# Optimization experiments

Measured on AMD Instinct MI355X. Metric: run time of the kernel, lower is better.

## Reference

```python
import jax, jax.numpy as jnp
import numpy as np

N_NODES = 50000
N_GRAPHS = 64
HID = 100

def gcn_conv(x, W, b, src, dst, n):
    # dense transform first (PyG GCNConv): [N, out]
    h = x @ W
    # add self loops (improved=False -> fill 1.0)
    loops = jnp.arange(n, dtype=src.dtype)
    s = jnp.concatenate([src, loops])
    d = jnp.concatenate([dst, loops])
    # symmetric normalization D^-1/2 A D^-1/2
    deg = jax.ops.segment_sum(jnp.ones_like(s, dtype=h.dtype), d, num_segments=n)
    dinv = jnp.where(deg > 0, jax.lax.rsqrt(jnp.maximum(deg, 1e-12)), 0.0)
    norm = dinv[s] * dinv[d]  # [E+N]
    msgs = h[s] * norm[:, None]  # gather + scale
    out = jax.ops.segment_sum(msgs, d, num_segments=n)  # scatter-add
    return out + b

def global_mean_pool(x, batch, num_graphs):
    sums = jax.ops.segment_sum(x, batch, num_segments=num_graphs)
    cnts = jax.ops.segment_sum(jnp.ones((x.shape[0],), x.dtype), batch, num_segments=num_graphs)
    return sums / jnp.maximum(cnts, 1.0)[:, None]

def setup_inputs() -> dict:
    key = jax.random.key(0)
    ks = jax.random.split(key, 8)
    d_in = 128
    x = jax.random.normal(ks[0], (N_NODES, d_in), dtype=jnp.float32)
    edge_index = jax.random.randint(ks[1], (2, 800000), 0, N_NODES, dtype=jnp.int64)
    batch = jnp.sort(jax.random.randint(ks[2], (N_NODES,), 0, N_GRAPHS, dtype=jnp.int64))
    s1 = 1.0 / np.sqrt(d_in)
    s2 = 1.0 / np.sqrt(HID)
    W1 = jax.random.uniform(ks[3], (d_in, HID), jnp.float32, -s1, s1)
    b1 = jnp.zeros((HID,), jnp.float32)
    W2 = jax.random.uniform(ks[4], (HID, HID), jnp.float32, -s2, s2)
    b2 = jnp.zeros((HID,), jnp.float32)
    Wlin = jax.random.uniform(ks[5], (HID, 1), jnp.float32, -s2, s2)
    blin = jax.random.uniform(ks[6], (1,), jnp.float32, -s2, s2)
    return {"x": x, "edge_index": edge_index, "batch": batch,
            "W1": W1, "b1": b1, "W2": W2, "b2": b2, "Wlin": Wlin, "blin": blin}

def reference(x, edge_index, batch, W1, b1, W2, b2, Wlin, blin):
    src, dst = edge_index[0], edge_index[1]
    h = gcn_conv(x, W1, b1, src, dst, N_NODES)
    h = jnp.tanh(h)
    h = gcn_conv(h, W2, b2, src, dst, N_NODES)
    g = global_mean_pool(h, batch, N_GRAPHS)  # [G, HID]
    return g @ Wlin + blin  # [G, 1]
```

## Files before the change

### kernel.cpp

```cpp
#include <hip/hip_runtime.h>
#include <hip/hip_bf16.h>

#define N_NODES 50000
#define N_GRAPHS 64
#define HID 100
#define HP 104

#define BKE  4096
#define NBIN 196
#define MAXBLK 256

#define NPB 39

#define OFF_DINV 0
#define OFF_CNTF 50048
#define OFF_POOL 50112
#define OFF_WT1  50176
#define OFF_HS   64512
#define OFF_ROWPTR 7864512
#define OFF_EIDX   7914560
#define OFF_BE     8714560
#define OFF_BBINS  9514560
#define OFF_BOFF   9565760
#define OFF_BTOT   9616960
#define OFF_BBASE  9617216
#define OFF_W2L    9617472
#define OFF_Q      9617600

typedef __attribute__((ext_vector_type(8))) short short8;
typedef __attribute__((ext_vector_type(4))) float floatx4;

__device__ inline float b2f(unsigned int u) {
    union { unsigned int v; float f; } x; x.v = u << 16; return x.f;
}
__device__ inline unsigned short f2b(float f) {
    union { float f; unsigned int v; } x; x.f = f;
    unsigned int r = (x.v + 0x7fffu + ((x.v >> 16) & 1u)) >> 16;
    return (unsigned short)r;
}

__global__ __launch_bounds__(256) void k_prep(const float* __restrict__ W1,
                                              const float* __restrict__ W2,
                                              const float* __restrict__ Wlin,
                                              const float* __restrict__ b2,
                                              unsigned short* __restrict__ Wt1,
                                              float* __restrict__ w2l,
                                              float* __restrict__ pool,
                                              float* __restrict__ cntf) {
    const int b = blockIdx.x, t = threadIdx.x;
    if (b < 56) {
        int idx = b * 256 + t;
        int c = idx >> 7, k = idx & 127;
        float v = (k < 128 && c < HID) ? W1[k * HID + c] : 0.0f;
        Wt1[c * 128 + k] = f2b(v);
    } else {
        if (t < 104) {
            float s = 0.0f;
            if (t < 100)
                for (int c = 0; c < HID; ++c) s += W2[t * HID + c] * Wlin[c];
            w2l[t] = s;
        } else if (t == 104) {
            float s = 0.0f;
            for (int j = 0; j < HID; ++j) s += b2[j] * Wlin[j];
            w2l[104] = s;
        } else if (t >= 128 && t < 128 + N_GRAPHS) {
            pool[t - 128] = 0.0f; cntf[t - 128] = 0.0f;
        }
    }
}

__global__ __launch_bounds__(256) void k_p1(const int* __restrict__ dst, int E,
                                            int* __restrict__ bbins) {
    __shared__ int hist[256];
    const int t = threadIdx.x, b = blockIdx.x;
    hist[t] = 0;
    __syncthreads();
    int e0 = b * BKE, e1 = min(e0 + BKE, E);
    for (int e = e0 + t; e < e1; e += 256) atomicAdd(&hist[dst[e] >> 8], 1);
    __syncthreads();
    if (t < NBIN) bbins[b * NBIN + t] = hist[t];
}

__global__ __launch_bounds__(256) void k_p2a(const int* __restrict__ bbins, int nb,
                                             int* __restrict__ boff, int* __restrict__ btot) {
    __shared__ int sb[256];
    const int t = threadIdx.x, j = blockIdx.x;
    int v = (t < nb) ? bbins[t * NBIN + j] : 0;
    sb[t] = v;
    __syncthreads();
    for (int off = 1; off < 256; off <<= 1) {
        int u = (t >= off) ? sb[t - off] : 0;
        __syncthreads();
        sb[t] += u;
        __syncthreads();
    }
    if (t < nb) boff[t * NBIN + j] = sb[t] - v;
    if (t == 255) btot[j] = sb[255];
}

__global__ __launch_bounds__(256) void k_p2b(const int* __restrict__ btot, int E,
                                             int* __restrict__ bbase, int* __restrict__ rowptr) {
    __shared__ int sb[256];
    const int t = threadIdx.x;
    int v = (t < NBIN) ? btot[t] : 0;
    sb[t] = v;
    __syncthreads();
    for (int off = 1; off < 256; off <<= 1) {
        int u = (t >= off) ? sb[t - off] : 0;
        __syncthreads();
        sb[t] += u;
        __syncthreads();
    }
    if (t < NBIN) bbase[t] = sb[t] - v;
    if (t == 0) { bbase[NBIN] = E; rowptr[N_NODES] = E; }
}

__global__ __launch_bounds__(256) void k_p3(const int* __restrict__ src, const int* __restrict__ dst,
                                            int E, const int* __restrict__ boff,
                                            const int* __restrict__ bbase,
                                            unsigned int* __restrict__ bE) {
    __shared__ unsigned int stage[BKE];
    __shared__ int hist[256], pref[256], cur[256], sb[256], offr[NBIN];
    const int t = threadIdx.x, b = blockIdx.x;
    hist[t] = 0;
    if (t < NBIN) offr[t] = boff[b * NBIN + t] + bbase[t];
    __syncthreads();
    const int e0 = b * BKE, e1 = min(e0 + BKE, E), n = e1 - e0;
    unsigned int mine[16];
#pragma unroll
    for (int u = 0; u < 16; ++u) {
        int e = e0 + u * 256 + t;
        if (e < e1) {
            unsigned int v = ((unsigned int)src[e] << 16) | (unsigned int)dst[e];
            mine[u] = v;
            atomicAdd(&hist[(v >> 8) & 255], 1);
        }
    }
    __syncthreads();
    sb[t] = hist[t];
    __syncthreads();
    for (int off = 1; off < 256; off <<= 1) {
        int v = (t >= off) ? sb[t - off] : 0;
        __syncthreads();
        sb[t] += v;
        __syncthreads();
    }
    pref[t] = sb[t] - hist[t];
    cur[t] = pref[t];
    __syncthreads();
#pragma unroll
    for (int u = 0; u < 16; ++u) {
        int e = e0 + u * 256 + t;
        if (e < e1) {
            unsigned int v = mine[u];
            int p = atomicAdd(&cur[(v >> 8) & 255], 1);
            stage[p] = v;
        }
    }
    __syncthreads();
    for (int i = t; i < n; i += 256) {
        unsigned int v = stage[i];
        int bin = (v >> 8) & 255;
        bE[offr[bin] + (i - pref[bin])] = v;
    }
}

__global__ __launch_bounds__(256) void k_p4(const unsigned int* __restrict__ bE,
                                            const int* __restrict__ bbase,
                                            int* __restrict__ rowptr, unsigned short* __restrict__ eidx,
                                            float* __restrict__ dinv) {
    __shared__ int hist[256], pref[256], cur[256], sb[256];
    const int t = threadIdx.x, b = blockIdx.x;
    const int eBase = bbase[b], eEnd = bbase[b + 1], n = eEnd - eBase;
    hist[t] = 0;
    __syncthreads();
    for (int i = t; i < n; i += 256) atomicAdd(&hist[bE[eBase + i] & 255], 1);
    __syncthreads();
    sb[t] = hist[t];
    __syncthreads();
    for (int off = 1; off < 256; off <<= 1) {
        int v = (t >= off) ? sb[t - off] : 0;
        __syncthreads();
        sb[t] += v;
        __syncthreads();
    }
    pref[t] = sb[t] - hist[t];
    cur[t] = pref[t];
    int node = (b << 8) + t;
    if (node < N_NODES) {
        rowptr[node] = eBase + pref[t];
        dinv[node] = rsqrtf((float)(hist[t] + 1));
    }
    __syncthreads();
    for (int i = t; i < n; i += 256) {
        unsigned int v = bE[eBase + i];
        int p = atomicAdd(&cur[v & 255], 1);
        eidx[eBase + p] = (unsigned short)(v >> 16);
    }
}

__global__ __launch_bounds__(256) void k_gemm(const float* __restrict__ A,
                                              const unsigned short* __restrict__ Wt,
                                              const float* __restrict__ dinv,
                                              unsigned short* __restrict__ out) {
    __shared__ __align__(16) unsigned short xs[64][136];
    __shared__ __align__(16) unsigned short ws[112][136];
    const int t = threadIdx.x;
    const int base = blockIdx.x * 64;

    for (int idx = t; idx < 112 * 64; idx += 256) {
        int c = idx >> 6, u = idx & 63;
        *(unsigned int*)&ws[c][2 * u] = ((const unsigned int*)Wt)[idx];
    }
    for (int idx = t; idx < 64 * 32; idx += 256) {
        int r = idx >> 5, q = idx & 31;
        int row = base + r;
        ushort4 p;
        if (row < N_NODES) {
            float4 v = ((const float4*)(A + (size_t)row * 128))[q];
            p.x = f2b(v.x); p.y = f2b(v.y); p.z = f2b(v.z); p.w = f2b(v.w);
        } else p = make_ushort4(0, 0, 0, 0);
        *(ushort4*)&xs[r][4 * q] = p;
    }
    __syncthreads();

    const int lane = t & 63, w = t >> 6;
    const int g = lane >> 4, cl = lane & 15;

    floatx4 acc[7];
#pragma unroll
    for (int n = 0; n < 7; ++n) acc[n] = (floatx4){0.f, 0.f, 0.f, 0.f};

#pragma unroll
    for (int kc = 0; kc < 4; ++kc) {
        short8 a = *(const short8*)&xs[w * 16 + cl][kc * 32 + 8 * g];
#pragma unroll
        for (int n = 0; n < 7; ++n) {
            short8 b = *(const short8*)&ws[n * 16 + cl][kc * 32 + 8 * g];
            acc[n] = __builtin_amdgcn_mfma_f32_16x16x32_bf16(a, b, acc[n], 0, 0, 0);
        }
    }

    float di[4]; int grows[4];
#pragma unroll
    for (int r = 0; r < 4; ++r) {
        grows[r] = base + w * 16 + 4 * g + r;
        di[r] = (grows[r] < N_NODES) ? dinv[grows[r]] : 0.0f;
    }
#pragma unroll
    for (int n = 0; n < 7; ++n) {
        int gcol = n * 16 + cl;
        if (gcol >= HP) continue;
#pragma unroll
        for (int r = 0; r < 4; ++r) {
            if (grows[r] < N_NODES)
                out[(size_t)grows[r] * HP + gcol] = f2b(acc[n][r] * di[r]);
        }
    }
}

#define ACC8(v) do { \
    s[0] += b2f((v).x & 0xffff); s[1] += b2f((v).x >> 16); \
    s[2] += b2f((v).y & 0xffff); s[3] += b2f((v).y >> 16); \
    s[4] += b2f((v).z & 0xffff); s[5] += b2f((v).z >> 16); \
    s[6] += b2f((v).w & 0xffff); s[7] += b2f((v).w >> 16); } while (0)

__global__ __launch_bounds__(512) void k_gather_q(const int* __restrict__ rowptr,
                                                  const unsigned short* __restrict__ eidx,
                                                  const unsigned short* __restrict__ hs,
                                                  const float* __restrict__ dinv,
                                                  const float* __restrict__ b1,
                                                  const float* __restrict__ w2l,
                                                  float* __restrict__ q) {
    __shared__ float wl[104];
    __shared__ float bsh[104];
    __shared__ float part[512];
    const int t = threadIdx.x;
    if (t < 104) { wl[t] = w2l[t]; bsh[t] = (t < 100) ? b1[t] : 0.0f; }
    const int nid = t / 13, c = t - nid * 13;
    const int i = blockIdx.x * NPB + nid;
    const bool active = (t < NPB * 13) && (i < N_NODES);
    __syncthreads();

    float partial = 0.0f;
    float di = 0.0f;
    if (active) {
        const int c0 = 8 * c;
        float s[8] = {0.f, 0.f, 0.f, 0.f, 0.f, 0.f, 0.f, 0.f};
        uint4 sv = *(const uint4*)(hs + (size_t)i * HP + c0);
        ACC8(sv);
        int e = rowptr[i];
        const int end = rowptr[i + 1];
        for (; e + 16 <= end; e += 16) {
            int n[16];
#pragma unroll
            for (int u = 0; u < 16; ++u) n[u] = eidx[e + u];
            uint4 v[16];
#pragma unroll
            for (int u = 0; u < 16; ++u) v[u] = *(const uint4*)(hs + (size_t)n[u] * HP + c0);
#pragma unroll
            for (int u = 0; u < 16; ++u) ACC8(v[u]);
        }
        for (; e + 8 <= end; e += 8) {
            int n[8];
#pragma unroll
            for (int u = 0; u < 8; ++u) n[u] = eidx[e + u];
            uint4 v[8];
#pragma unroll
            for (int u = 0; u < 8; ++u) v[u] = *(const uint4*)(hs + (size_t)n[u] * HP + c0);
#pragma unroll
            for (int u = 0; u < 8; ++u) ACC8(v[u]);
        }
        for (; e + 4 <= end; e += 4) {
            int n[4];
#pragma unroll
            for (int u = 0; u < 4; ++u) n[u] = eidx[e + u];
            uint4 v[4];
#pragma unroll
            for (int u = 0; u < 4; ++u) v[u] = *(const uint4*)(hs + (size_t)n[u] * HP + c0);
#pragma unroll
            for (int u = 0; u < 4; ++u) ACC8(v[u]);
        }
        for (; e < end; ++e) {
            uint4 v = *(const uint4*)(hs + (size_t)eidx[e] * HP + c0);
            ACC8(v);
        }
        di = dinv[i];
#pragma unroll
        for (int j = 0; j < 8; ++j) {
            float h = tanhf(di * s[j] + bsh[c0 + j]);
            partial += h * wl[c0 + j];
        }
    }
    part[t] = partial;
    __syncthreads();
    if (active && c == 0) {
        float sum = 0.0f;
#pragma unroll
        for (int j = 0; j < 13; ++j) sum += part[t + j];
        q[i] = di * sum;
    }
}

__global__ __launch_bounds__(256) void k_gpool(const int* __restrict__ rowptr,
                                               const unsigned short* __restrict__ eidx,
                                               const float* __restrict__ q,
                                               const float* __restrict__ dinv,
                                               const int* __restrict__ batch,
                                               float* __restrict__ pool,
                                               float* __restrict__ cntf) {
    __shared__ float sp[N_GRAPHS];
    __shared__ float sc[N_GRAPHS];
    const int t = threadIdx.x;
    if (t < N_GRAPHS) { sp[t] = 0.0f; sc[t] = 0.0f; }
    __syncthreads();
    int i = blockIdx.x * 256 + t;
    if (i < N_NODES) {
        float s = q[i];
        int e = rowptr[i];
        const int end = rowptr[i + 1];
        for (; e + 8 <= end; e += 8) {
            int n0 = eidx[e],     n1 = eidx[e + 1], n2 = eidx[e + 2], n3 = eidx[e + 3];
            int n4 = eidx[e + 4], n5 = eidx[e + 5], n6 = eidx[e + 6], n7 = eidx[e + 7];
            s += q[n0] + q[n1] + q[n2] + q[n3] + q[n4] + q[n5] + q[n6] + q[n7];
        }
        for (; e + 4 <= end; e += 4) {
            int n0 = eidx[e], n1 = eidx[e + 1], n2 = eidx[e + 2], n3 = eidx[e + 3];
            s += q[n0] + q[n1] + q[n2] + q[n3];
        }
        for (; e < end; ++e) s += q[eidx[e]];
        float p = dinv[i] * s;
        int g = batch[i];
        atomicAdd(&sp[g], p);
        atomicAdd(&sc[g], 1.0f);
    }
    __syncthreads();
    if (t < N_GRAPHS && sc[t] != 0.0f) {
        atomicAdd(&pool[t], sp[t]);
        atomicAdd(&cntf[t], sc[t]);
    }
}

__global__ void k_final(const float* __restrict__ pool, const float* __restrict__ cnt,
                        const float* __restrict__ w2l, const float* __restrict__ blin,
                        float* __restrict__ out) {
    int g = threadIdx.x;
    if (g >= N_GRAPHS) return;
    out[g] = pool[g] / fmaxf(cnt[g], 1.0f) + w2l[104] + blin[0];
}

extern "C" void kernel_launch(void* const* d_in, const int* in_sizes, int n_in,
                              void* d_out, int out_size, void* d_ws, size_t ws_size,
                              hipStream_t stream) {
    const float* x    = (const float*)d_in[0];
    const int*   ei   = (const int*)d_in[1];
    const int*   batch= (const int*)d_in[2];
    const float* W1   = (const float*)d_in[3];
    const float* b1   = (const float*)d_in[4];
    const float* W2   = (const float*)d_in[5];
    const float* b2   = (const float*)d_in[6];
    const float* Wlin = (const float*)d_in[7];
    const float* blin = (const float*)d_in[8];
    float* out = (float*)d_out;

    const int E = in_sizes[1] / 2;
    const int* src = ei;
    const int* dst = ei + E;

    float* wsf  = (float*)d_ws;
    int*   wsi  = (int*)d_ws;
    float* dinv = wsf + OFF_DINV;
    float* cntf = wsf + OFF_CNTF;
    float* pool = wsf + OFF_POOL;
    unsigned short* Wt1 = (unsigned short*)(wsf + OFF_WT1);
    unsigned short* HS  = (unsigned short*)(wsf + OFF_HS);
    int* rowptr = wsi + OFF_ROWPTR;
    unsigned short* eidx = (unsigned short*)(wsi + OFF_EIDX);
    unsigned int* bE = (unsigned int*)(wsi + OFF_BE);
    int* bbins  = wsi + OFF_BBINS;
    int* boff   = wsi + OFF_BOFF;
    int* btot   = wsi + OFF_BTOT;
    int* bbase  = wsi + OFF_BBASE;
    float* w2l  = wsf + OFF_W2L;
    float* q    = wsf + OFF_Q;

    const int nbE = (E + BKE - 1) / BKE;
    const int nGrid = (N_NODES + 255) / 256;
    const int gqGrid = (N_NODES + NPB - 1) / NPB;

    k_prep<<<57, 256, 0, stream>>>(W1, W2, Wlin, b2, Wt1, w2l, pool, cntf);
    k_p1<<<nbE, 256, 0, stream>>>(dst, E, bbins);
    k_p2a<<<NBIN, 256, 0, stream>>>(bbins, nbE, boff, btot);
    k_p2b<<<1, 256, 0, stream>>>(btot, E, bbase, rowptr);
    k_p3<<<nbE, 256, 0, stream>>>(src, dst, E, boff, bbase, bE);
    k_p4<<<NBIN, 256, 0, stream>>>(bE, bbase, rowptr, eidx, dinv);

    k_gemm<<<(N_NODES + 63) / 64, 256, 0, stream>>>(x, Wt1, dinv, HS);

    k_gather_q<<<gqGrid, 512, 0, stream>>>(rowptr, eidx, HS, dinv, b1, w2l, q);

    k_gpool<<<nGrid, 256, 0, stream>>>(rowptr, eidx, q, dinv, batch, pool, cntf);

    k_final<<<1, 64, 0, stream>>>(pool, cntf, w2l, blin, out);
}
```

Measured before the change: 106.8 us.

## Fuse CSR build into one cooperative kernel and fold final into pooling

Merges the weight prep and the four CSR-construction passes into a single cooperative kernel that uses grid-wide syncs between phases instead of separate launches. The final division step moves into the pooling kernel through a last-block ticket counter. This is meant to remove launch overhead and inter-kernel gaps across about seven small launches. In exchange it relies on all 196 blocks being co-resident, adds grid barrier cost, and assumes E/BKE equals NBIN (196 blocks) for the input size.

```diff
diff --git a/kernel.cpp b/kernel.cpp
--- a/kernel.cpp
+++ b/kernel.cpp
@@ -1,5 +1,8 @@
 #include <hip/hip_runtime.h>
 #include <hip/hip_bf16.h>
+#include <hip/hip_cooperative_groups.h>
+
+namespace cg = cooperative_groups;
 
 #define N_NODES 50000
 #define N_GRAPHS 64
@@ -8,8 +11,6 @@
 
 #define BKE  4096
 #define NBIN 196
-#define MAXBLK 256
-
 #define NPB 39
 
 #define OFF_DINV 0
@@ -23,7 +24,7 @@
 #define OFF_BBINS  9514560
 #define OFF_BOFF   9565760
 #define OFF_BTOT   9616960
-#define OFF_BBASE  9617216
+#define OFF_DONE   9617440
 #define OFF_W2L    9617472
 #define OFF_Q      9617600
 
@@ -39,21 +40,42 @@
     return (unsigned short)r;
 }
 
-__global__ __launch_bounds__(256) void k_prep(const float* __restrict__ W1,
-                                              const float* __restrict__ W2,
-                                              const float* __restrict__ Wlin,
-                                              const float* __restrict__ b2,
-                                              unsigned short* __restrict__ Wt1,
-                                              float* __restrict__ w2l,
-                                              float* __restrict__ pool,
-                                              float* __restrict__ cntf) {
-    const int b = blockIdx.x, t = threadIdx.x;
-    if (b < 56) {
+__global__ __launch_bounds__(256) void k_csr(const int* __restrict__ src,
+                                             const int* __restrict__ dst, int E,
+                                             const float* __restrict__ W1,
+                                             const float* __restrict__ W2,
+                                             const float* __restrict__ Wlin,
+                                             const float* __restrict__ b2,
+                                             unsigned short* __restrict__ Wt1,
+                                             float* __restrict__ w2l,
+                                             float* __restrict__ pool,
+                                             float* __restrict__ cntf,
+                                             int* __restrict__ done,
+                                             int* __restrict__ bbins,
+                                             int* __restrict__ boff,
+                                             int* __restrict__ btot,
+                                             unsigned int* __restrict__ bE,
+                                             int* __restrict__ rowptr,
+                                             unsigned short* __restrict__ eidx,
+                                             float* __restrict__ dinv) {
+    cg::grid_group grid = cg::this_grid();
+    __shared__ unsigned int stage[BKE];
+    __shared__ int hist[256], pref[256], cur[256], sb[256];
+    __shared__ int offr[NBIN];
+    __shared__ int bba[NBIN + 1];
+    const int t = threadIdx.x, b = blockIdx.x;
+    const int e0 = b * BKE, e1 = min(e0 + BKE, E);
+    unsigned int mine[16];
+
+    {
         int idx = b * 256 + t;
-        int c = idx >> 7, k = idx & 127;
-        float v = (k < 128 && c < HID) ? W1[k * HID + c] : 0.0f;
-        Wt1[c * 128 + k] = f2b(v);
-    } else {
+        if (idx < 112 * 128) {
+            int c = idx >> 7, k = idx & 127;
+            float v = (c < HID) ? W1[k * HID + c] : 0.0f;
+            Wt1[c * 128 + k] = f2b(v);
+        }
+    }
+    if (b == NBIN - 1) {
         if (t < 104) {
             float s = 0.0f;
             if (t < 100)
@@ -65,68 +87,12 @@
             w2l[104] = s;
         } else if (t >= 128 && t < 128 + N_GRAPHS) {
             pool[t - 128] = 0.0f; cntf[t - 128] = 0.0f;
-        }
-    }
-}
-
-__global__ __launch_bounds__(256) void k_p1(const int* __restrict__ dst, int E,
-                                            int* __restrict__ bbins) {
-    __shared__ int hist[256];
-    const int t = threadIdx.x, b = blockIdx.x;
+        } else if (t == 224) {
+            *done = 0;
+        }
+    }
     hist[t] = 0;
     __syncthreads();
-    int e0 = b * BKE, e1 = min(e0 + BKE, E);
-    for (int e = e0 + t; e < e1; e += 256) atomicAdd(&hist[dst[e] >> 8], 1);
-    __syncthreads();
-    if (t < NBIN) bbins[b * NBIN + t] = hist[t];
-}
-
-__global__ __launch_bounds__(256) void k_p2a(const int* __restrict__ bbins, int nb,
-                                             int* __restrict__ boff, int* __restrict__ btot) {
-    __shared__ int sb[256];
-    const int t = threadIdx.x, j = blockIdx.x;
-    int v = (t < nb) ? bbins[t * NBIN + j] : 0;
-    sb[t] = v;
-    __syncthreads();
-    for (int off = 1; off < 256; off <<= 1) {
-        int u = (t >= off) ? sb[t - off] : 0;
-        __syncthreads();
-        sb[t] += u;
-        __syncthreads();
-    }
-    if (t < nb) boff[t * NBIN + j] = sb[t] - v;
-    if (t == 255) btot[j] = sb[255];
-}
-
-__global__ __launch_bounds__(256) void k_p2b(const int* __restrict__ btot, int E,
-                                             int* __restrict__ bbase, int* __restrict__ rowptr) {
-    __shared__ int sb[256];
-    const int t = threadIdx.x;
-    int v = (t < NBIN) ? btot[t] : 0;
-    sb[t] = v;
-    __syncthreads();
-    for (int off = 1; off < 256; off <<= 1) {
-        int u = (t >= off) ? sb[t - off] : 0;
-        __syncthreads();
-        sb[t] += u;
-        __syncthreads();
-    }
-    if (t < NBIN) bbase[t] = sb[t] - v;
-    if (t == 0) { bbase[NBIN] = E; rowptr[N_NODES] = E; }
-}
-
-__global__ __launch_bounds__(256) void k_p3(const int* __restrict__ src, const int* __restrict__ dst,
-                                            int E, const int* __restrict__ boff,
-                                            const int* __restrict__ bbase,
-                                            unsigned int* __restrict__ bE) {
-    __shared__ unsigned int stage[BKE];
-    __shared__ int hist[256], pref[256], cur[256], sb[256], offr[NBIN];
-    const int t = threadIdx.x, b = blockIdx.x;
-    hist[t] = 0;
-    if (t < NBIN) offr[t] = boff[b * NBIN + t] + bbase[t];
-    __syncthreads();
-    const int e0 = b * BKE, e1 = min(e0 + BKE, E), n = e1 - e0;
-    unsigned int mine[16];
 #pragma unroll
     for (int u = 0; u < 16; ++u) {
         int e = e0 + u * 256 + t;
@@ -137,65 +103,95 @@
         }
     }
     __syncthreads();
-    sb[t] = hist[t];
-    __syncthreads();
-    for (int off = 1; off < 256; off <<= 1) {
-        int v = (t >= off) ? sb[t - off] : 0;
-        __syncthreads();
-        sb[t] += v;
-        __syncthreads();
-    }
-    pref[t] = sb[t] - hist[t];
-    cur[t] = pref[t];
-    __syncthreads();
-#pragma unroll
-    for (int u = 0; u < 16; ++u) {
-        int e = e0 + u * 256 + t;
-        if (e < e1) {
-            unsigned int v = mine[u];
-            int p = atomicAdd(&cur[(v >> 8) & 255], 1);
-            stage[p] = v;
-        }
-    }
-    __syncthreads();
-    for (int i = t; i < n; i += 256) {
-        unsigned int v = stage[i];
-        int bin = (v >> 8) & 255;
-        bE[offr[bin] + (i - pref[bin])] = v;
-    }
-}
-
-__global__ __launch_bounds__(256) void k_p4(const unsigned int* __restrict__ bE,
-                                            const int* __restrict__ bbase,
-                                            int* __restrict__ rowptr, unsigned short* __restrict__ eidx,
-                                            float* __restrict__ dinv) {
-    __shared__ int hist[256], pref[256], cur[256], sb[256];
-    const int t = threadIdx.x, b = blockIdx.x;
-    const int eBase = bbase[b], eEnd = bbase[b + 1], n = eEnd - eBase;
-    hist[t] = 0;
-    __syncthreads();
-    for (int i = t; i < n; i += 256) atomicAdd(&hist[bE[eBase + i] & 255], 1);
-    __syncthreads();
-    sb[t] = hist[t];
-    __syncthreads();
-    for (int off = 1; off < 256; off <<= 1) {
-        int v = (t >= off) ? sb[t - off] : 0;
-        __syncthreads();
-        sb[t] += v;
-        __syncthreads();
-    }
-    pref[t] = sb[t] - hist[t];
-    cur[t] = pref[t];
-    int node = (b << 8) + t;
-    if (node < N_NODES) {
-        rowptr[node] = eBase + pref[t];
-        dinv[node] = rsqrtf((float)(hist[t] + 1));
-    }
-    __syncthreads();
-    for (int i = t; i < n; i += 256) {
-        unsigned int v = bE[eBase + i];
-        int p = atomicAdd(&cur[v & 255], 1);
-        eidx[eBase + p] = (unsigned short)(v >> 16);
+    if (t < NBIN) bbins[b * NBIN + t] = hist[t];
+    grid.sync();
+
+    {
+        int v = (t < NBIN) ? bbins[t * NBIN + b] : 0;
+        sb[t] = v;
+        __syncthreads();
+        for (int off = 1; off < 256; off <<= 1) {
+            int u = (t >= off) ? sb[t - off] : 0;
+            __syncthreads();
+            sb[t] += u;
+            __syncthreads();
+        }
+        if (t < NBIN) boff[t * NBIN + b] = sb[t] - v;
+        if (t == 255) btot[b] = sb[255];
+    }
+    grid.sync();
+
+    {
+        int v = (t < NBIN) ? btot[t] : 0;
+        sb[t] = v;
+        __syncthreads();
+        for (int off = 1; off < 256; off <<= 1) {
+            int u = (t >= off) ? sb[t - off] : 0;
+            __syncthreads();
+            sb[t] += u;
+            __syncthreads();
+        }
+        if (t < NBIN) bba[t] = sb[t] - v;
+        if (t == 0) { bba[NBIN] = E; rowptr[N_NODES] = E; }
+        __syncthreads();
+        if (t < NBIN) offr[t] = boff[b * NBIN + t] + bba[t];
+        sb[t] = hist[t];
+        __syncthreads();
+        for (int off = 1; off < 256; off <<= 1) {
+            int u = (t >= off) ? sb[t - off] : 0;
+            __syncthreads();
+            sb[t] += u;
+            __syncthreads();
+        }
+        pref[t] = sb[t] - hist[t];
+        cur[t] = pref[t];
+        __syncthreads();
+#pragma unroll
+        for (int u = 0; u < 16; ++u) {
+            int e = e0 + u * 256 + t;
+            if (e < e1) {
+                unsigned int v = mine[u];
+                int p = atomicAdd(&cur[(v >> 8) & 255], 1);
+                stage[p] = v;
+            }
+        }
+        __syncthreads();
+        const int n = e1 - e0;
+        for (int i = t; i < n; i += 256) {
+            unsigned int v = stage[i];
+            int bin = (v >> 8) & 255;
+            bE[offr[bin] + (i - pref[bin])] = v;
+        }
+    }
+    grid.sync();
+
+    {
+        const int eBase = bba[b], eEnd = bba[b + 1], n = eEnd - eBase;
+        hist[t] = 0;
+        __syncthreads();
+        for (int i = t; i < n; i += 256) atomicAdd(&hist[bE[eBase + i] & 255], 1);
+        __syncthreads();
+        sb[t] = hist[t];
+        __syncthreads();
+        for (int off = 1; off < 256; off <<= 1) {
+            int u = (t >= off) ? sb[t - off] : 0;
+            __syncthreads();
+            sb[t] += u;
+            __syncthreads();
+        }
+        pref[t] = sb[t] - hist[t];
+        cur[t] = pref[t];
+        int node = (b << 8) + t;
+        if (node < N_NODES) {
+            rowptr[node] = eBase + pref[t];
+            dinv[node] = rsqrtf((float)(hist[t] + 1));
+        }
+        __syncthreads();
+        for (int i = t; i < n; i += 256) {
+            unsigned int v = bE[eBase + i];
+            int p = atomicAdd(&cur[v & 255], 1);
+            eidx[eBase + p] = (unsigned short)(v >> 16);
+        }
     }
 }
 
@@ -348,9 +344,14 @@
                                                const float* __restrict__ dinv,
                                                const int* __restrict__ batch,
                                                float* __restrict__ pool,
-                                               float* __restrict__ cntf) {
+                                               float* __restrict__ cntf,
+                                               const float* __restrict__ w2l,
+                                               const float* __restrict__ blin,
+                                               int* __restrict__ done,
+                                               float* __restrict__ out) {
     __shared__ float sp[N_GRAPHS];
     __shared__ float sc[N_GRAPHS];
+    __shared__ int lastFlag;
     const int t = threadIdx.x;
     if (t < N_GRAPHS) { sp[t] = 0.0f; sc[t] = 0.0f; }
     __syncthreads();
@@ -379,14 +380,18 @@
         atomicAdd(&pool[t], sp[t]);
         atomicAdd(&cntf[t], sc[t]);
     }
-}
-
-__global__ void k_final(const float* __restrict__ pool, const float* __restrict__ cnt,
-                        const float* __restrict__ w2l, const float* __restrict__ blin,
-                        float* __restrict__ out) {
-    int g = threadIdx.x;
-    if (g >= N_GRAPHS) return;
-    out[g] = pool[g] / fmaxf(cnt[g], 1.0f) + w2l[104] + blin[0];
+    __syncthreads();
+    if (t == 0) {
+        __threadfence();
+        int ticket = atomicAdd(done, 1);
+        lastFlag = (ticket == (int)gridDim.x - 1);
+    }
+    __syncthreads();
+    if (lastFlag && t < N_GRAPHS) {
+        float p = atomicAdd(&pool[t], 0.0f);
+        float c = atomicAdd(&cntf[t], 0.0f);
+        out[t] = p / fmaxf(c, 1.0f) + w2l[104] + blin[0];
+    }
 }
 
 extern "C" void kernel_launch(void* const* d_in, const int* in_sizes, int n_in,
@@ -403,7 +408,7 @@
     const float* blin = (const float*)d_in[8];
     float* out = (float*)d_out;
 
-    const int E = in_sizes[1] / 2;
+    int E = in_sizes[1] / 2;
     const int* src = ei;
     const int* dst = ei + E;
 
@@ -420,26 +425,26 @@
     int* bbins  = wsi + OFF_BBINS;
     int* boff   = wsi + OFF_BOFF;
     int* btot   = wsi + OFF_BTOT;
-    int* bbase  = wsi + OFF_BBASE;
+    int* done   = wsi + OFF_DONE;
     float* w2l  = wsf + OFF_W2L;
     float* q    = wsf + OFF_Q;
 
-    const int nbE = (E + BKE - 1) / BKE;
     const int nGrid = (N_NODES + 255) / 256;
     const int gqGrid = (N_NODES + NPB - 1) / NPB;
 
-    k_prep<<<57, 256, 0, stream>>>(W1, W2, Wlin, b2, Wt1, w2l, pool, cntf);
-    k_p1<<<nbE, 256, 0, stream>>>(dst, E, bbins);
-    k_p2a<<<NBIN, 256, 0, stream>>>(bbins, nbE, boff, btot);
-    k_p2b<<<1, 256, 0, stream>>>(btot, E, bbase, rowptr);
-    k_p3<<<nbE, 256, 0, stream>>>(src, dst, E, boff, bbase, bE);
-    k_p4<<<NBIN, 256, 0, stream>>>(bE, bbase, rowptr, eidx, dinv);
+    void* csrArgs[] = {
+        (void*)&src, (void*)&dst, (void*)&E,
+        (void*)&W1, (void*)&W2, (void*)&Wlin, (void*)&b2,
+        (void*)&Wt1, (void*)&w2l, (void*)&pool, (void*)&cntf, (void*)&done,
+        (void*)&bbins, (void*)&boff, (void*)&btot, (void*)&bE,
+        (void*)&rowptr, (void*)&eidx, (void*)&dinv
+    };
+    hipLaunchCooperativeKernel((void*)k_csr, dim3(NBIN), dim3(256), csrArgs, 0, stream);
 
     k_gemm<<<(N_NODES + 63) / 64, 256, 0, stream>>>(x, Wt1, dinv, HS);
 
     k_gather_q<<<gqGrid, 512, 0, stream>>>(rowptr, eidx, HS, dinv, b1, w2l, q);
 
-    k_gpool<<<nGrid, 256, 0, stream>>>(rowptr, eidx, q, dinv, batch, pool, cntf);
-
-    k_final<<<1, 64, 0, stream>>>(pool, cntf, w2l, blin, out);
-}
+    k_gpool<<<nGrid, 256, 0, stream>>>(rowptr, eidx, q, dinv, batch, pool, cntf,
+                                       w2l, blin, done, out);
+}
```

Result: slower. 174.0 us (+62.9%).
